# Performance work log

Measured on AMD Instinct MI355X. Metric: run time of the kernel, lower is better.

The kernel has to match this reference:

```python
import jax, jax.numpy as jnp
import numpy as np

NUM_EXPERTS = 8


def setup_inputs() -> dict:
    key = jax.random.key(0)
    k1, k2, k3, k4 = jax.random.split(key, 4)
    d_model, d_ff, E = 768, 3072, NUM_EXPERTS
    B, S = 4, 1024
    scale_in = 1.0 / np.sqrt(d_model)
    scale_ff = 1.0 / np.sqrt(d_ff)
    return {
        "hidden_states": jax.random.normal(k1, (B, S, d_model), dtype=jnp.float32),
        "router_weight": jax.random.normal(k2, (d_model, E), dtype=jnp.float32) * scale_in,
        "wi": jax.random.normal(k3, (E, d_model, d_ff), dtype=jnp.float32) * scale_in,
        "wo": jax.random.normal(k4, (E, d_ff, d_model), dtype=jnp.float32) * scale_ff,
    }


def reference(hidden_states, router_weight, wi, wo):
    # --- Top-1 router (HF computes softmax in fp32) ---
    router_logits = jnp.einsum("bsd,de->bse", hidden_states.astype(jnp.float32), router_weight.astype(jnp.float32))  # [B,S,E]
    probs = jax.nn.softmax(router_logits, axis=-1)
    expert_index = jnp.argmax(probs, axis=-1)                      # [B,S] int
    router_mask = jax.nn.one_hot(expert_index, NUM_EXPERTS, dtype=probs.dtype)  # [B,S,E]
    router_probs = jnp.max(probs, axis=-1, keepdims=True).astype(hidden_states.dtype)  # [B,S,1]

    # --- Experts: dense per-expert MLP, combined by the one-hot top-1 mask.
    # Every token is routed to exactly one expert, so masked-sum == dispatch/combine.
    h = jax.nn.relu(jnp.einsum("bsd,edf->bsef", hidden_states, wi))  # [B,S,E,d_ff]
    y = jnp.einsum("bsef,efd->bsed", h, wo)                           # [B,S,E,d_model]
    next_states = jnp.einsum("bse,bsed->bsd", router_mask.astype(hidden_states.dtype), y)

    out = router_probs * next_states
    return out, router_logits, expert_index
```

## Files before the change

kernel.cpp:

```cpp
#include <hip/hip_runtime.h>


typedef __attribute__((ext_vector_type(4))) float f32x4;
typedef __attribute__((ext_vector_type(8))) short short8;
typedef unsigned short ushort_t;
typedef unsigned int uint32;

#define DEVFN static __device__ __forceinline__
#define MFMA __builtin_amdgcn_mfma_f32_16x16x32_bf16

constexpr int NTOK = 4096;
constexpr int DM   = 768;
constexpr int DF   = 3072;
constexpr int NE   = 8;
constexpr int TM   = 128;
constexpr int MAXTILES = NTOK / TM + NE;
constexpr int MAXR  = MAXTILES * TM;
constexpr int BK    = 32;
constexpr int NKT   = 768 / BK;

DEVFN ushort_t f2bf(float f) {
  uint32 u = __float_as_uint(f);
  u += 0x7fffu + ((u >> 16) & 1u);
  return (ushort_t)(u >> 16);
}
DEVFN float bf2f(ushort_t u) { return __uint_as_float((uint32)u << 16); }

DEVFN void gl16(const void* g, void* l) {
  __builtin_amdgcn_global_load_lds(
      (const __attribute__((address_space(1))) void*)g,
      (__attribute__((address_space(3))) void*)l, 16, 0, 0);
}

__global__ __launch_bounds__(256) void k_router(
    const float* __restrict__ X, const float* __restrict__ Wr,
    float* __restrict__ out_logits, float* __restrict__ out_idx,
    int* __restrict__ expert_of, float* __restrict__ prob) {
  int wid = threadIdx.x >> 6, lane = threadIdx.x & 63;
  int t = blockIdx.x * 4 + wid;
  const float* xrow = X + (size_t)t * DM;
  double acc[NE];
#pragma unroll
  for (int e = 0; e < NE; e++) acc[e] = 0.0;
  for (int d0 = 0; d0 < DM; d0 += 64) {
    int d = d0 + lane;
    float x = xrow[d];
    const float4* w4 = (const float4*)(Wr + (size_t)d * NE);
    float4 wa = w4[0], wb = w4[1];
    acc[0] += (double)x * wa.x; acc[1] += (double)x * wa.y;
    acc[2] += (double)x * wa.z; acc[3] += (double)x * wa.w;
    acc[4] += (double)x * wb.x; acc[5] += (double)x * wb.y;
    acc[6] += (double)x * wb.z; acc[7] += (double)x * wb.w;
  }
#pragma unroll
  for (int e = 0; e < NE; e++) {
#pragma unroll
    for (int s = 32; s > 0; s >>= 1) acc[e] += __shfl_xor(acc[e], s);
  }
#pragma unroll
  for (int e = 0; e < NE; e++)
    if (lane == e) out_logits[(size_t)t * NE + e] = (float)acc[e];
  double m = acc[0]; int idx = 0;
#pragma unroll
  for (int e = 1; e < NE; e++) if (acc[e] > m) { m = acc[e]; idx = e; }
  float s = 0.f;
#pragma unroll
  for (int e = 0; e < NE; e++) s += expf((float)(acc[e] - m));
  if (lane == 0) {
    out_idx[t] = (float)idx;
    expert_of[t] = idx;
    prob[t] = 1.f / s;
  }
}

__global__ __launch_bounds__(64) void k_scan(
    const int* __restrict__ expert_of, const float* __restrict__ prob,
    int* __restrict__ meta, int* __restrict__ perm,
    float* __restrict__ prob_g) {
  __shared__ int exl[NTOK];
  int lane = threadIdx.x;
  const int4* src = (const int4*)expert_of;
  int4* dst = (int4*)exl;
#pragma unroll
  for (int j = 0; j < NTOK / 4 / 64; j++) dst[j * 64 + lane] = src[j * 64 + lane];
  __syncthreads();
  int cnt[NE];
#pragma unroll
  for (int e = 0; e < NE; e++) cnt[e] = 0;
  for (int j = 0; j < 64; j++) {
    int ex = exl[lane * 64 + j];
#pragma unroll
    for (int e = 0; e < NE; e++) cnt[e] += (ex == e);
  }
  int base[NE], tot[NE];
#pragma unroll
  for (int e = 0; e < NE; e++) {
    int inc = cnt[e];
#pragma unroll
    for (int s = 1; s < 64; s <<= 1) {
      int o = __shfl_up(inc, s);
      if (lane >= s) inc += o;
    }
    base[e] = inc - cnt[e];
    tot[e] = __shfl(inc, 63);
  }
  int segStart[NE];
  int pos = 0, nt = 0;
#pragma unroll
  for (int e = 0; e < NE; e++) {
    segStart[e] = pos;
    int tiles = (tot[e] + TM - 1) / TM;
    if (lane == 0) {
      meta[8 + e] = pos;
      meta[16 + e] = pos + tot[e];
      for (int i = 0; i < tiles; i++) {
        meta[64 + nt + i] = e;
        meta[128 + nt + i] = pos + i * TM;
      }
    }
    nt += tiles;
    pos += tiles * TM;
  }
  if (lane == 0) meta[24] = nt;
  int cum[NE];
#pragma unroll
  for (int e = 0; e < NE; e++) cum[e] = segStart[e] + base[e];
  for (int j = 0; j < 64; j++) {
    int t = lane * 64 + j;
    int ex = exl[lane * 64 + j];
    int p = 0;
#pragma unroll
    for (int e = 0; e < NE; e++) p += (ex == e) ? cum[e] : 0;
#pragma unroll
    for (int e = 0; e < NE; e++) cum[e] += (ex == e);
    perm[p] = t;
    prob_g[p] = prob[t];
  }
}

__global__ __launch_bounds__(256) void k_copy(
    const float* __restrict__ X, const int* __restrict__ meta,
    const int* __restrict__ perm, ushort_t* __restrict__ Xg) {
  int bt = blockIdx.y;
  if (bt >= meta[24]) return;
  int e = meta[64 + bt], row0 = meta[128 + bt], segEnd = meta[16 + e];
  int wid = threadIdx.x >> 6, lane = threadIdx.x & 63;
  int r = row0 + blockIdx.x * 4 + wid;
  if (r >= segEnd) return;
  int tok = perm[r];
  const float2* s2 = (const float2*)(X + (size_t)tok * DM);
  uint32* d2 = (uint32*)(Xg + (size_t)r * DM);
#pragma unroll
  for (int i = 0; i < DM / 128; i++) {
    float2 v = s2[i * 64 + lane];
    d2[i * 64 + lane] = (uint32)f2bf(v.x) | ((uint32)f2bf(v.y) << 16);
  }
}

__global__ __launch_bounds__(256) void k_convT(
    const float* __restrict__ W, ushort_t* __restrict__ WT, int R, int C) {
  __shared__ ushort_t T[128 * 128];
  int e = blockIdx.z;
  int r0 = blockIdx.x * 128, c0 = blockIdx.y * 128;
  const float* src = W + ((size_t)e * R + r0) * C + c0;
  int t = threadIdx.x;
  int rr = t >> 5, cc = (t & 31) * 4;
#pragma unroll
  for (int j = 0; j < 16; j++) {
    int r = rr + j * 8;
    float4 v = *(const float4*)(src + (size_t)r * C + cc);
#pragma unroll
    for (int i = 0; i < 4; i++) {
      int c = cc + i;
      T[c * 128 + (((r >> 3) ^ (c & 15)) << 3) + (r & 7)] =
          f2bf(((const float*)&v)[i]);
    }
  }
  __syncthreads();
  int q = t & 15, cb = t >> 4;
#pragma unroll
  for (int j = 0; j < 8; j++) {
    int c = cb + j * 16;
    short8 v = *(const short8*)&T[c * 128 + ((q ^ (c & 15)) << 3)];
    *(short8*)(WT + ((size_t)e * C + c0 + c) * R + r0 + q * 8) = v;
  }
}

template <int LDA, int NB, bool FIRST>
__global__ __launch_bounds__(256, 2) void k_gemm8(
    const ushort_t* __restrict__ A, const ushort_t* __restrict__ BT,
    const int* __restrict__ meta, ushort_t* __restrict__ Obf) {
  __shared__ short A_lds[4][128 * BK];
  __shared__ short B_lds[4][128 * BK];

  int bt = blockIdx.y;
  if (bt >= meta[24]) return;
  int e    = meta[64 + bt];
  int row0 = meta[128 + bt];
  int n0, koff, z;
  if constexpr (FIRST) {
    n0 = blockIdx.x * 128; koff = 0; z = 0;
  } else {
    n0 = (blockIdx.x >> 2) * 128; z = blockIdx.x & 3; koff = z * 768;
  }

  int tid = threadIdx.x, lane = tid & 63, w = tid >> 6;
  int wr = w >> 1, wc = w & 1;

  int srcSlot = (lane & 3) ^ ((lane >> 3) & 3);
  const ushort_t* aS = A + (size_t)(row0 + (tid >> 2)) * LDA + koff + srcSlot * 8;
  const ushort_t* bS = BT + ((size_t)e * NB + n0 + (tid >> 2)) * LDA + koff + srcSlot * 8;
  int dstOff = w * 512;

#define STAGE(sl, kt)                                                        \
  do {                                                                       \
    gl16(aS + (size_t)(kt) * BK, &A_lds[sl][dstOff]);                        \
    gl16(aS + (size_t)(kt) * BK + (size_t)64 * LDA, &A_lds[sl][dstOff + 2048]); \
    gl16(bS + (size_t)(kt) * BK, &B_lds[sl][dstOff]);                        \
    gl16(bS + (size_t)(kt) * BK + (size_t)64 * LDA, &B_lds[sl][dstOff + 2048]); \
  } while (0)

  int kslotRd = ((lane >> 4) ^ ((lane >> 1) & 3)) * 8;
  int aOff[4], bOff[4];
#pragma unroll
  for (int m = 0; m < 4; m++)
    aOff[m] = (wr * 64 + m * 16 + (lane & 15)) * BK + kslotRd;
#pragma unroll
  for (int n = 0; n < 4; n++)
    bOff[n] = (wc * 64 + n * 16 + (lane & 15)) * BK + kslotRd;

  f32x4 acc[4][4];
#pragma unroll
  for (int m = 0; m < 4; m++)
#pragma unroll
    for (int n = 0; n < 4; n++) acc[m][n] = (f32x4){0.f, 0.f, 0.f, 0.f};

  STAGE(0, 0); STAGE(1, 1); STAGE(2, 2);

#pragma unroll 4
  for (int t = 0; t < NKT; ++t) {
    __builtin_amdgcn_sched_barrier(0);
    asm volatile("s_waitcnt vmcnt(8)" ::: "memory");
    __builtin_amdgcn_s_barrier();
    asm volatile("" ::: "memory");
    __builtin_amdgcn_sched_barrier(0);
    int tp = (t + 3 < NKT) ? t + 3 : t;
    STAGE((t + 3) & 3, tp);
    const short* aB = A_lds[t & 3];
    const short* bB = B_lds[t & 3];
    short8 af[4], bf[4];
#pragma unroll
    for (int m = 0; m < 4; m++) af[m] = *(const short8*)&aB[aOff[m]];
#pragma unroll
    for (int n = 0; n < 4; n++) bf[n] = *(const short8*)&bB[bOff[n]];
    __builtin_amdgcn_s_setprio(1);
#pragma unroll
    for (int m = 0; m < 4; m++)
#pragma unroll
      for (int n = 0; n < 4; n++)
        acc[m][n] = MFMA(af[m], bf[n], acc[m][n], 0, 0, 0);
    __builtin_amdgcn_s_setprio(0);
  }
#undef STAGE

  ushort_t* dst = FIRST ? Obf : Obf + (size_t)z * MAXR * NB;
#pragma unroll
  for (int m = 0; m < 4; m++) {
    int rowb = row0 + wr * 64 + m * 16 + (lane >> 4) * 4;
#pragma unroll
    for (int n = 0; n < 4; n++) {
      int col = n0 + wc * 64 + n * 16 + (lane & 15);
#pragma unroll
      for (int r = 0; r < 4; r++) {
        float v = acc[m][n][r];
        if (FIRST) v = v > 0.f ? v : 0.f;
        dst[(size_t)(rowb + r) * NB + col] = f2bf(v);
      }
    }
  }
}

__global__ __launch_bounds__(256) void k_reduce(
    const ushort_t* __restrict__ P, const int* __restrict__ meta,
    const int* __restrict__ perm, const float* __restrict__ prob_g,
    float* __restrict__ out) {
  int bt = blockIdx.y;
  if (bt >= meta[24]) return;
  int e = meta[64 + bt], row0 = meta[128 + bt], segEnd = meta[16 + e];
  int c0 = blockIdx.x * 64;
  int t = threadIdx.x;
  int col = c0 + (t & 7) * 8;
#pragma unroll
  for (int i = 0; i < 4; i++) {
    int r = row0 + (t >> 3) + i * 32;
    if (r >= segEnd) continue;
    int tok = perm[r];
    float p = prob_g[r];
    float s[8];
#pragma unroll
    for (int j = 0; j < 8; j++) s[j] = 0.f;
#pragma unroll
    for (int z = 0; z < 4; z++) {
      short8 v = *(const short8*)&P[((size_t)z * MAXR + r) * DM + col];
#pragma unroll
      for (int j = 0; j < 8; j++) s[j] += bf2f((ushort_t)v[j]);
    }
    float4 o0 = {p * s[0], p * s[1], p * s[2], p * s[3]};
    float4 o1 = {p * s[4], p * s[5], p * s[6], p * s[7]};
    *(float4*)&out[(size_t)tok * DM + col] = o0;
    *(float4*)&out[(size_t)tok * DM + col + 4] = o1;
  }
}

extern "C" void kernel_launch(void* const* d_in, const int* in_sizes, int n_in,
                              void* d_out, int out_size, void* d_ws, size_t ws_size,
                              hipStream_t stream) {
  const float* X  = (const float*)d_in[0];
  const float* Wr = (const float*)d_in[1];
  const float* wi = (const float*)d_in[2];
  const float* wo = (const float*)d_in[3];

  float* out        = (float*)d_out;
  float* out_logits = out + (size_t)NTOK * DM;
  float* out_idx    = out_logits + (size_t)NTOK * NE;

  char* w = (char*)d_ws;
  int*      meta      = (int*)w;
  int*      expert_of = (int*)(w + 4096);
  float*    prob      = (float*)(w + 20480);
  int*      perm      = (int*)(w + 36864);
  float*    prob_g    = (float*)(w + 61440);
  ushort_t* Xg        = (ushort_t*)(w + 131072);
  ushort_t* H         = Xg + (size_t)MAXR * DM;
  ushort_t* woT       = H + (size_t)MAXR * DF;
  ushort_t* wiT       = woT + (size_t)NE * DM * DF;
  ushort_t* P         = wiT;

  k_convT<<<dim3(DM / 128, DF / 128, NE), 256, 0, stream>>>(wi, wiT, DM, DF);
  k_convT<<<dim3(DF / 128, DM / 128, NE), 256, 0, stream>>>(wo, woT, DF, DM);
  k_router<<<NTOK / 4, 256, 0, stream>>>(X, Wr, out_logits, out_idx,
                                         expert_of, prob);
  k_scan<<<1, 64, 0, stream>>>(expert_of, prob, meta, perm, prob_g);
  k_copy<<<dim3(TM / 4, MAXTILES), 256, 0, stream>>>(X, meta, perm, Xg);
  k_gemm8<DM, DF, true><<<dim3(DF / 128, MAXTILES), 256, 0, stream>>>(
      Xg, wiT, meta, H);
  k_gemm8<DF, DM, false><<<dim3((DM / 128) * 4, MAXTILES), 256, 0, stream>>>(
      H, woT, meta, P);
  k_reduce<<<dim3(DM / 64, MAXTILES), 256, 0, stream>>>(P, meta, perm, prob_g, out);
}
```

Baseline: 161.7 us.

## Use 3-stage LDS pipeline, 3 blocks/CU, and halve split-K in second GEMM

The GEMM kernel's LDS ring buffer drops from four stages to three, so launch bounds now request three resident blocks per CU. The main loop is restructured with a STEP macro: it skips staging past the end, and the last iteration waits on all loads instead of loading redundant tiles. The down-projection GEMM now uses split-K of 2 instead of 4. Each block in that GEMM therefore runs a longer K loop, and the reduce kernel reads half as many partials. The trade-off is less prefetch depth and fewer blocks in the second GEMM, in exchange for higher occupancy and less partial-sum traffic.

Measured after the change: 159.8 us. About the same (-1.1%).

```diff
diff --git a/kernel.cpp b/kernel.cpp
--- a/kernel.cpp
+++ b/kernel.cpp
@@ -17,7 +17,7 @@
 constexpr int MAXTILES = NTOK / TM + NE;
 constexpr int MAXR  = MAXTILES * TM;
 constexpr int BK    = 32;
-constexpr int NKT   = 768 / BK;
+constexpr int KS2   = 2;
 
 DEVFN ushort_t f2bf(float f) {
   uint32 u = __float_as_uint(f);
@@ -186,12 +186,13 @@
   }
 }
 
-template <int LDA, int NB, bool FIRST>
-__global__ __launch_bounds__(256, 2) void k_gemm8(
+template <int LDA, int NB, int KSPLIT, bool FIRST>
+__global__ __launch_bounds__(256, 3) void k_gemm8(
     const ushort_t* __restrict__ A, const ushort_t* __restrict__ BT,
     const int* __restrict__ meta, ushort_t* __restrict__ Obf) {
-  __shared__ short A_lds[4][128 * BK];
-  __shared__ short B_lds[4][128 * BK];
+  constexpr int NKTT = LDA / KSPLIT / BK;
+  __shared__ short A_lds[3][128 * BK];
+  __shared__ short B_lds[3][128 * BK];
 
   int bt = blockIdx.y;
   if (bt >= meta[24]) return;
@@ -201,7 +202,8 @@
   if constexpr (FIRST) {
     n0 = blockIdx.x * 128; koff = 0; z = 0;
   } else {
-    n0 = (blockIdx.x >> 2) * 128; z = blockIdx.x & 3; koff = z * 768;
+    n0 = (blockIdx.x / KSPLIT) * 128; z = blockIdx.x % KSPLIT;
+    koff = z * (LDA / KSPLIT);
   }
 
   int tid = threadIdx.x, lane = tid & 63, w = tid >> 6;
@@ -235,32 +237,34 @@
 #pragma unroll
     for (int n = 0; n < 4; n++) acc[m][n] = (f32x4){0.f, 0.f, 0.f, 0.f};
 
-  STAGE(0, 0); STAGE(1, 1); STAGE(2, 2);
-
-#pragma unroll 4
-  for (int t = 0; t < NKT; ++t) {
-    __builtin_amdgcn_sched_barrier(0);
-    asm volatile("s_waitcnt vmcnt(8)" ::: "memory");
-    __builtin_amdgcn_s_barrier();
-    asm volatile("" ::: "memory");
-    __builtin_amdgcn_sched_barrier(0);
-    int tp = (t + 3 < NKT) ? t + 3 : t;
-    STAGE((t + 3) & 3, tp);
-    const short* aB = A_lds[t & 3];
-    const short* bB = B_lds[t & 3];
-    short8 af[4], bf[4];
-#pragma unroll
-    for (int m = 0; m < 4; m++) af[m] = *(const short8*)&aB[aOff[m]];
-#pragma unroll
-    for (int n = 0; n < 4; n++) bf[n] = *(const short8*)&bB[bOff[n]];
-    __builtin_amdgcn_s_setprio(1);
-#pragma unroll
-    for (int m = 0; m < 4; m++)
-#pragma unroll
-      for (int n = 0; n < 4; n++)
-        acc[m][n] = MFMA(af[m], bf[n], acc[m][n], 0, 0, 0);
-    __builtin_amdgcn_s_setprio(0);
-  }
+  STAGE(0, 0); STAGE(1, 1);
+
+#define STEP(T, VMSTR)                                                       \
+  do {                                                                       \
+    __builtin_amdgcn_sched_barrier(0);                                       \
+    asm volatile("s_waitcnt vmcnt(" VMSTR ")" ::: "memory");                 \
+    __builtin_amdgcn_s_barrier();                                            \
+    asm volatile("" ::: "memory");                                           \
+    __builtin_amdgcn_sched_barrier(0);                                       \
+    if ((T) + 2 < NKTT) STAGE(((T) + 2) % 3, (T) + 2);                       \
+    const short* aB = A_lds[(T) % 3];                                        \
+    const short* bB = B_lds[(T) % 3];                                        \
+    short8 af[4], bf[4];                                                     \
+    _Pragma("unroll") for (int m = 0; m < 4; m++)                            \
+      af[m] = *(const short8*)&aB[aOff[m]];                                  \
+    _Pragma("unroll") for (int n = 0; n < 4; n++)                            \
+      bf[n] = *(const short8*)&bB[bOff[n]];                                  \
+    __builtin_amdgcn_s_setprio(1);                                           \
+    _Pragma("unroll") for (int m = 0; m < 4; m++)                            \
+      _Pragma("unroll") for (int n = 0; n < 4; n++)                          \
+        acc[m][n] = MFMA(af[m], bf[n], acc[m][n], 0, 0, 0);                  \
+    __builtin_amdgcn_s_setprio(0);                                           \
+  } while (0)
+
+#pragma unroll 3
+  for (int t = 0; t < NKTT - 1; ++t) STEP(t, "4");
+  STEP(NKTT - 1, "0");
+#undef STEP
 #undef STAGE
 
   ushort_t* dst = FIRST ? Obf : Obf + (size_t)z * MAXR * NB;
@@ -300,7 +304,7 @@
 #pragma unroll
     for (int j = 0; j < 8; j++) s[j] = 0.f;
 #pragma unroll
-    for (int z = 0; z < 4; z++) {
+    for (int z = 0; z < KS2; z++) {
       short8 v = *(const short8*)&P[((size_t)z * MAXR + r) * DM + col];
 #pragma unroll
       for (int j = 0; j < 8; j++) s[j] += bf2f((ushort_t)v[j]);
@@ -342,9 +346,9 @@
                                          expert_of, prob);
   k_scan<<<1, 64, 0, stream>>>(expert_of, prob, meta, perm, prob_g);
   k_copy<<<dim3(TM / 4, MAXTILES), 256, 0, stream>>>(X, meta, perm, Xg);
-  k_gemm8<DM, DF, true><<<dim3(DF / 128, MAXTILES), 256, 0, stream>>>(
+  k_gemm8<DM, DF, 1, true><<<dim3(DF / 128, MAXTILES), 256, 0, stream>>>(
       Xg, wiT, meta, H);
-  k_gemm8<DF, DM, false><<<dim3((DM / 128) * 4, MAXTILES), 256, 0, stream>>>(
+  k_gemm8<DF, DM, KS2, false><<<dim3((DM / 128) * KS2, MAXTILES), 256, 0, stream>>>(
       H, woT, meta, P);
   k_reduce<<<dim3(DM / 64, MAXTILES), 256, 0, stream>>>(P, meta, perm, prob_g, out);
 }
```

## Fuse fp32 weight conversion into grouped GEMMs, dropping separate transpose kernels

Applied to the files above, without the earlier changes.

Removes the two k_convT launches that converted and transposed wi/wo into bf16 buffers. The GEMMs now read the fp32 weights directly through registers, truncate-pack them to bf16 and write them into a padded, swizzled LDS layout. The pipeline drops from 4-stage async LDS staging to double buffering with __syncthreads, and occupancy is raised to 3 blocks. The second GEMM's split-K goes from 4 to 2, which halves the partial buffers the reduce has to read. In exchange, weight bytes read per tile double and each tile re-converts the weights. Rounding changes from round-to-nearest to truncation.

Measured after the change: 151.1 us. -6.5%, faster.

```diff
diff --git a/kernel.cpp b/kernel.cpp
--- a/kernel.cpp
+++ b/kernel.cpp
@@ -17,7 +17,8 @@
 constexpr int MAXTILES = NTOK / TM + NE;
 constexpr int MAXR  = MAXTILES * TM;
 constexpr int BK    = 32;
-constexpr int NKT   = 768 / BK;
+constexpr int KS2   = 2;
+constexpr int BSTR  = 40;
 
 DEVFN ushort_t f2bf(float f) {
   uint32 u = __float_as_uint(f);
@@ -25,6 +26,9 @@
   return (ushort_t)(u >> 16);
 }
 DEVFN float bf2f(ushort_t u) { return __uint_as_float((uint32)u << 16); }
+DEVFN uint32 pkbf(float a, float b) {
+  return (__float_as_uint(b) & 0xffff0000u) | (__float_as_uint(a) >> 16);
+}
 
 DEVFN void gl16(const void* g, void* l) {
   __builtin_amdgcn_global_load_lds(
@@ -157,41 +161,13 @@
   }
 }
 
-__global__ __launch_bounds__(256) void k_convT(
-    const float* __restrict__ W, ushort_t* __restrict__ WT, int R, int C) {
-  __shared__ ushort_t T[128 * 128];
-  int e = blockIdx.z;
-  int r0 = blockIdx.x * 128, c0 = blockIdx.y * 128;
-  const float* src = W + ((size_t)e * R + r0) * C + c0;
-  int t = threadIdx.x;
-  int rr = t >> 5, cc = (t & 31) * 4;
-#pragma unroll
-  for (int j = 0; j < 16; j++) {
-    int r = rr + j * 8;
-    float4 v = *(const float4*)(src + (size_t)r * C + cc);
-#pragma unroll
-    for (int i = 0; i < 4; i++) {
-      int c = cc + i;
-      T[c * 128 + (((r >> 3) ^ (c & 15)) << 3) + (r & 7)] =
-          f2bf(((const float*)&v)[i]);
-    }
-  }
-  __syncthreads();
-  int q = t & 15, cb = t >> 4;
-#pragma unroll
-  for (int j = 0; j < 8; j++) {
-    int c = cb + j * 16;
-    short8 v = *(const short8*)&T[c * 128 + ((q ^ (c & 15)) << 3)];
-    *(short8*)(WT + ((size_t)e * C + c0 + c) * R + r0 + q * 8) = v;
-  }
-}
-
-template <int LDA, int NB, bool FIRST>
-__global__ __launch_bounds__(256, 2) void k_gemm8(
-    const ushort_t* __restrict__ A, const ushort_t* __restrict__ BT,
+template <int KTOT, int NB, int KSPLIT, bool FIRST>
+__global__ __launch_bounds__(256, 3) void k_gemm8(
+    const ushort_t* __restrict__ A, const float* __restrict__ Bw,
     const int* __restrict__ meta, ushort_t* __restrict__ Obf) {
-  __shared__ short A_lds[4][128 * BK];
-  __shared__ short B_lds[4][128 * BK];
+  constexpr int NKTT = KTOT / KSPLIT / BK;
+  __shared__ short A_lds[2][128 * BK];
+  __shared__ short B_lds[2][128 * BSTR];
 
   int bt = blockIdx.y;
   if (bt >= meta[24]) return;
@@ -201,23 +177,47 @@
   if constexpr (FIRST) {
     n0 = blockIdx.x * 128; koff = 0; z = 0;
   } else {
-    n0 = (blockIdx.x >> 2) * 128; z = blockIdx.x & 3; koff = z * 768;
+    n0 = (blockIdx.x / KSPLIT) * 128; z = blockIdx.x % KSPLIT;
+    koff = z * (KTOT / KSPLIT);
   }
 
   int tid = threadIdx.x, lane = tid & 63, w = tid >> 6;
   int wr = w >> 1, wc = w & 1;
 
   int srcSlot = (lane & 3) ^ ((lane >> 3) & 3);
-  const ushort_t* aS = A + (size_t)(row0 + (tid >> 2)) * LDA + koff + srcSlot * 8;
-  const ushort_t* bS = BT + ((size_t)e * NB + n0 + (tid >> 2)) * LDA + koff + srcSlot * 8;
+  const ushort_t* aS = A + (size_t)(row0 + (tid >> 2)) * KTOT + koff + srcSlot * 8;
   int dstOff = w * 512;
 
-#define STAGE(sl, kt)                                                        \
-  do {                                                                       \
-    gl16(aS + (size_t)(kt) * BK, &A_lds[sl][dstOff]);                        \
-    gl16(aS + (size_t)(kt) * BK + (size_t)64 * LDA, &A_lds[sl][dstOff + 2048]); \
-    gl16(bS + (size_t)(kt) * BK, &B_lds[sl][dstOff]);                        \
-    gl16(bS + (size_t)(kt) * BK + (size_t)64 * LDA, &B_lds[sl][dstOff + 2048]); \
+#define STAGE_A(buf, kt)                                                      \
+  do {                                                                        \
+    gl16(aS + (size_t)(kt) * BK, &A_lds[buf][dstOff]);                        \
+    gl16(aS + (size_t)(kt) * BK + (size_t)64 * KTOT,                          \
+         &A_lds[buf][dstOff + 2048]);                                         \
+  } while (0)
+
+  int kq = tid >> 5, nb = tid & 31;
+  const float* bS = Bw + (size_t)e * KTOT * NB + ((size_t)koff + kq * 4) * NB
+                    + n0 + nb * 4;
+  float4 bv0, bv1, bv2, bv3;
+
+#define LOAD_B(kt)                                                            \
+  do {                                                                        \
+    const float* b0 = bS + (size_t)(kt) * BK * NB;                            \
+    bv0 = *(const float4*)(b0);                                               \
+    bv1 = *(const float4*)(b0 + NB);                                          \
+    bv2 = *(const float4*)(b0 + 2 * NB);                                      \
+    bv3 = *(const float4*)(b0 + 3 * NB);                                      \
+  } while (0)
+
+#define WRITE_B(buf)                                                          \
+  do {                                                                        \
+    _Pragma("unroll") for (int nn = 0; nn < 4; nn++) {                        \
+      int n = nb * 4 + nn;                                                    \
+      uint32 w0 = pkbf(((const float*)&bv0)[nn], ((const float*)&bv1)[nn]);   \
+      uint32 w1 = pkbf(((const float*)&bv2)[nn], ((const float*)&bv3)[nn]);   \
+      uint2* wp = (uint2*)&B_lds[buf][n * BSTR + ((kq ^ (n & 6)) << 2)];      \
+      *wp = (uint2){w0, w1};                                                  \
+    }                                                                         \
   } while (0)
 
   int kslotRd = ((lane >> 4) ^ ((lane >> 1) & 3)) * 8;
@@ -226,8 +226,10 @@
   for (int m = 0; m < 4; m++)
     aOff[m] = (wr * 64 + m * 16 + (lane & 15)) * BK + kslotRd;
 #pragma unroll
-  for (int n = 0; n < 4; n++)
-    bOff[n] = (wc * 64 + n * 16 + (lane & 15)) * BK + kslotRd;
+  for (int n = 0; n < 4; n++) {
+    int col = wc * 64 + n * 16 + (lane & 15);
+    bOff[n] = col * BSTR + (((lane >> 4) * 2) ^ (col & 6)) * 4;
+  }
 
   f32x4 acc[4][4];
 #pragma unroll
@@ -235,19 +237,20 @@
 #pragma unroll
     for (int n = 0; n < 4; n++) acc[m][n] = (f32x4){0.f, 0.f, 0.f, 0.f};
 
-  STAGE(0, 0); STAGE(1, 1); STAGE(2, 2);
-
-#pragma unroll 4
-  for (int t = 0; t < NKT; ++t) {
-    __builtin_amdgcn_sched_barrier(0);
-    asm volatile("s_waitcnt vmcnt(8)" ::: "memory");
-    __builtin_amdgcn_s_barrier();
-    asm volatile("" ::: "memory");
-    __builtin_amdgcn_sched_barrier(0);
-    int tp = (t + 3 < NKT) ? t + 3 : t;
-    STAGE((t + 3) & 3, tp);
-    const short* aB = A_lds[t & 3];
-    const short* bB = B_lds[t & 3];
+  LOAD_B(0);
+  STAGE_A(0, 0);
+  WRITE_B(0);
+  __syncthreads();
+
+#pragma unroll 2
+  for (int t = 0; t < NKTT; ++t) {
+    int cur = t & 1;
+    if (t + 1 < NKTT) {
+      LOAD_B(t + 1);
+      STAGE_A(cur ^ 1, t + 1);
+    }
+    const short* aB = A_lds[cur];
+    const short* bB = B_lds[cur];
     short8 af[4], bf[4];
 #pragma unroll
     for (int m = 0; m < 4; m++) af[m] = *(const short8*)&aB[aOff[m]];
@@ -260,8 +263,12 @@
       for (int n = 0; n < 4; n++)
         acc[m][n] = MFMA(af[m], bf[n], acc[m][n], 0, 0, 0);
     __builtin_amdgcn_s_setprio(0);
-  }
-#undef STAGE
+    if (t + 1 < NKTT) WRITE_B(cur ^ 1);
+    __syncthreads();
+  }
+#undef STAGE_A
+#undef LOAD_B
+#undef WRITE_B
 
   ushort_t* dst = FIRST ? Obf : Obf + (size_t)z * MAXR * NB;
 #pragma unroll
@@ -300,7 +307,7 @@
 #pragma unroll
     for (int j = 0; j < 8; j++) s[j] = 0.f;
 #pragma unroll
-    for (int z = 0; z < 4; z++) {
+    for (int z = 0; z < KS2; z++) {
       short8 v = *(const short8*)&P[((size_t)z * MAXR + r) * DM + col];
 #pragma unroll
       for (int j = 0; j < 8; j++) s[j] += bf2f((ushort_t)v[j]);
@@ -332,19 +339,15 @@
   float*    prob_g    = (float*)(w + 61440);
   ushort_t* Xg        = (ushort_t*)(w + 131072);
   ushort_t* H         = Xg + (size_t)MAXR * DM;
-  ushort_t* woT       = H + (size_t)MAXR * DF;
-  ushort_t* wiT       = woT + (size_t)NE * DM * DF;
-  ushort_t* P         = wiT;
-
-  k_convT<<<dim3(DM / 128, DF / 128, NE), 256, 0, stream>>>(wi, wiT, DM, DF);
-  k_convT<<<dim3(DF / 128, DM / 128, NE), 256, 0, stream>>>(wo, woT, DF, DM);
+  ushort_t* P         = H + (size_t)MAXR * DF;
+
   k_router<<<NTOK / 4, 256, 0, stream>>>(X, Wr, out_logits, out_idx,
                                          expert_of, prob);
   k_scan<<<1, 64, 0, stream>>>(expert_of, prob, meta, perm, prob_g);
   k_copy<<<dim3(TM / 4, MAXTILES), 256, 0, stream>>>(X, meta, perm, Xg);
-  k_gemm8<DM, DF, true><<<dim3(DF / 128, MAXTILES), 256, 0, stream>>>(
-      Xg, wiT, meta, H);
-  k_gemm8<DF, DM, false><<<dim3((DM / 128) * 4, MAXTILES), 256, 0, stream>>>(
-      H, woT, meta, P);
+  k_gemm8<DM, DF, 1, true><<<dim3(DF / 128, MAXTILES), 256, 0, stream>>>(
+      Xg, wi, meta, H);
+  k_gemm8<DF, DM, KS2, false><<<dim3((DM / 128) * KS2, MAXTILES), 256, 0, stream>>>(
+      H, wo, meta, P);
   k_reduce<<<dim3(DM / 64, MAXTILES), 256, 0, stream>>>(P, meta, perm, prob_g, out);
 }
```
